# Kernel tuning notes

Measured on AMD Instinct MI355X. Metric: run time of the kernel, lower is better.

## Reference

```python
import jax, jax.numpy as jnp
import numpy as np
import math

SCALE = math.sqrt(256.0)

def setup_inputs() -> dict:
    key = jax.random.key(0)
    k1, k2, k3, k4, k5 = jax.random.split(key, 5)
    B, C, T, D = 8, 80, 2048, 256
    bound = 1.0 / math.sqrt(C)
    x = jax.random.normal(k1, (B, C, T), dtype=jnp.float32)
    Wk = jax.random.uniform(k2, (D, C), minval=-bound, maxval=bound, dtype=jnp.float32)
    bk = jax.random.uniform(k3, (D,), minval=-bound, maxval=bound, dtype=jnp.float32)
    Wq = jax.random.uniform(k4, (D, C), minval=-bound, maxval=bound, dtype=jnp.float32)
    bq = jax.random.uniform(k5, (D,), minval=-bound, maxval=bound, dtype=jnp.float32)
    return {"x": x, "Wk": Wk, "bk": bk, "Wq": Wq, "bq": bq}

def reference(x, Wk, bk, Wq, bq):
    # x: [B, C=80, T]; work in time-major layout [B, T, C]
    xt = jnp.swapaxes(x, 1, 2)                      # [B, T, C]
    K = xt @ Wk.T + bk                              # [B, T, 256]
    Q = xt @ Wq.T + bq                              # [B, T, 256]
    # softmax over last dim (dim=2 in torch) of K Q^T / sqrt(256)
    att = jax.nn.softmax(jnp.einsum('bid,bjd->bij', K, Q) / SCALE, axis=2)
    # original per-timestep loop is exactly att @ xt (values = raw input, no V proj)
    out = jnp.einsum('bij,bjc->bic', att, xt)       # [B, T, C]
    return jnp.swapaxes(out, 1, 2)                  # [B, C, T]
```

## Files before the change

kernel.cpp:

```cpp
#include <hip/hip_runtime.h>
#include <hip/hip_bf16.h>
#include <math.h>

typedef __bf16 bf16;
typedef __bf16 bf16x8 __attribute__((ext_vector_type(8)));
typedef float  f32x4  __attribute__((ext_vector_type(4)));
typedef float  f32x16 __attribute__((ext_vector_type(16)));
typedef uint32_t u32x4 __attribute__((ext_vector_type(4)));

#define MFMA16(a, b, c) __builtin_amdgcn_mfma_f32_16x16x32_bf16((a), (b), (c), 0, 0, 0)
#define MFMA32(a, b, c) __builtin_amdgcn_mfma_f32_32x32x16_bf16((a), (b), (c), 0, 0, 0)

typedef const uint32_t __attribute__((address_space(1)))* gq_t;
typedef uint32_t __attribute__((address_space(3)))* lq_t;

constexpr int B_ = 8, C_ = 80, T_ = 2048, D_ = 256;
constexpr int NS = 4;
constexpr float LOG2E_16 = 0.090169989f;

static __device__ inline uint32_t pkbf(float lo, float hi) {
  bf16 l = (bf16)lo, h = (bf16)hi;
  uint16_t lb = __builtin_bit_cast(uint16_t, l), hb = __builtin_bit_cast(uint16_t, h);
  return (uint32_t)lb | ((uint32_t)hb << 16);
}

constexpr int VF_TILE = 3 * 2 * 2 * 32 * 8;

__global__ __launch_bounds__(256) void proj_kernel(
    const float* __restrict__ x,
    const float* __restrict__ Wk,
    const float* __restrict__ bk,
    const float* __restrict__ Wq,
    const float* __restrict__ bq,
    bf16* __restrict__ Kb,
    bf16* __restrict__ Qb,
    bf16* __restrict__ Vf)
{
  const int t0   = blockIdx.x * 32;
  const int b    = blockIdx.y;
  const int tid  = threadIdx.x;
  const int w    = tid >> 6;
  const int lane = tid & 63;
  const int h    = lane >> 4;
  const int lr   = lane & 15;

  const float* xb = x + (size_t)b * C_ * T_;

  {
    bf16* vout = Vf + (size_t)(b * 64 + blockIdx.x) * VF_TILE;
    #pragma unroll
    for (int g = 0; g < 2; ++g) {
      int f = tid + g * 256;
      if (f < 384) {
        int il2 = f & 31, hi2 = (f >> 5) & 1, kj2 = (f >> 6) & 1, cb2 = f >> 7;
        int c = cb2 * 32 + il2;
        bf16x8 o;
        if (c < 80) {
          const float* sp = xb + (size_t)c * T_ + t0 + kj2 * 16 + hi2 * 8;
          f32x4 v0 = *reinterpret_cast<const f32x4*>(sp);
          f32x4 v1 = *reinterpret_cast<const f32x4*>(sp + 4);
          #pragma unroll
          for (int e = 0; e < 4; ++e) { o[e] = (bf16)v0[e]; o[e + 4] = (bf16)v1[e]; }
        } else {
          #pragma unroll
          for (int e = 0; e < 8; ++e) o[e] = (bf16)0.f;
        }
        *reinterpret_cast<bf16x8*>(vout + f * 8) = o;
      }
    }
  }

  bf16x8 afrag[2][3];
  #pragma unroll
  for (int ib = 0; ib < 2; ++ib) {
    int t = t0 + ib * 16 + lr;
    #pragma unroll
    for (int ks = 0; ks < 3; ++ks) {
      bf16x8 v;
      #pragma unroll
      for (int e = 0; e < 8; ++e) {
        int c = ks * 32 + h * 8 + e;
        float val;
        if (c < 80)       val = xb[c * T_ + t];
        else if (c == 80) val = 1.0f;
        else              val = 0.0f;
        v[e] = (bf16)val;
      }
      afrag[ib][ks] = v;
    }
  }

  const int nb0 = w * 4;
  #pragma unroll
  for (int mat = 0; mat < 2; ++mat) {
    const float* W    = mat ? Wq : Wk;
    const float* bias = mat ? bq : bk;
    bf16* outp        = mat ? Qb : Kb;

    f32x4 acc[2][4];
    #pragma unroll
    for (int ib = 0; ib < 2; ++ib)
      #pragma unroll
      for (int nb = 0; nb < 4; ++nb)
        acc[ib][nb] = f32x4{0.f, 0.f, 0.f, 0.f};

    #pragma unroll
    for (int nb = 0; nb < 4; ++nb) {
      int d = (nb0 + nb) * 16 + lr;
      #pragma unroll
      for (int ks = 0; ks < 3; ++ks) {
        bf16x8 bv;
        #pragma unroll
        for (int e = 0; e < 8; ++e) {
          int c = ks * 32 + h * 8 + e;
          float val;
          if (c < 80)       val = W[d * C_ + c];
          else if (c == 80) val = bias[d];
          else              val = 0.0f;
          bv[e] = (bf16)val;
        }
        #pragma unroll
        for (int ib = 0; ib < 2; ++ib)
          acc[ib][nb] = MFMA16(afrag[ib][ks], bv, acc[ib][nb]);
      }
    }

    #pragma unroll
    for (int ib = 0; ib < 2; ++ib)
      #pragma unroll
      for (int nb = 0; nb < 4; ++nb) {
        int d = (nb0 + nb) * 16 + lr;
        #pragma unroll
        for (int r = 0; r < 4; ++r) {
          int t = t0 + ib * 16 + h * 4 + r;
          outp[(size_t)(b * T_ + t) * D_ + d] = (bf16)acc[ib][nb][r];
        }
      }
  }
}

__global__ __launch_bounds__(256, 2) void attn_kernel(
    const bf16* __restrict__ Kb,
    const bf16* __restrict__ Qb,
    const bf16* __restrict__ Vf,
    float* __restrict__ Opart,
    float* __restrict__ mpart,
    float* __restrict__ lpart)
{
  constexpr int BN = 32, NT = T_ / BN;
  constexpr int JT_PER = NT / NS;
  __shared__ bf16 qlds[2][BN * D_];
  __shared__ bf16 vlds[2][VF_TILE];

  const int flat = blockIdx.x;
  const int b    = flat & 7;
  const int rem  = flat >> 3;
  const int it   = rem & 15;
  const int s    = rem >> 4;
  const int i0   = it * 128;

  const int tid  = threadIdx.x;
  const int w    = tid >> 6;
  const int lane = tid & 63;
  const int il   = lane & 31;
  const int hi   = lane >> 5;
  const int iw   = i0 + w * 32;

  const bf16* Kbase = Kb + (size_t)b * T_ * D_;
  const bf16* Qbase = Qb + (size_t)b * T_ * D_;
  const bf16* Vbase = Vf + (size_t)b * 64 * VF_TILE;

  bf16x8 kf[16];
  {
    const bf16* kp = Kbase + (size_t)(iw + il) * D_ + hi * 8;
    #pragma unroll
    for (int ks = 0; ks < 16; ++ks)
      kf[ks] = *reinterpret_cast<const bf16x8*>(kp + ks * 16);
  }

  f32x16 oacc[3];
  #pragma unroll
  for (int cb = 0; cb < 3; ++cb)
    #pragma unroll
    for (int r = 0; r < 16; ++r) oacc[cb][r] = 0.f;
  float m_run = -INFINITY, l_run = 0.f;

  auto stage = [&](int jt, int buf) {
    #pragma unroll
    for (int q = 0; q < 4; ++q) {
      int f = tid + 256 * q;
      int j = f >> 5, c = f & 31;
      const bf16* src = Qbase + (size_t)(jt * BN + j) * D_ + ((c ^ j) << 3);
      __builtin_amdgcn_global_load_lds((gq_t)src,
          (lq_t)&qlds[buf][(q * 256 + w * 64) * 8], 16, 0, 0);
    }
    const bf16* vsrc = Vbase + (size_t)jt * VF_TILE;
    __builtin_amdgcn_global_load_lds((gq_t)(vsrc + (size_t)tid * 8),
        (lq_t)&vlds[buf][(w * 64) * 8], 16, 0, 0);
    if (w < 2)
      __builtin_amdgcn_global_load_lds((gq_t)(vsrc + (size_t)(256 + tid) * 8),
          (lq_t)&vlds[buf][(256 + w * 64) * 8], 16, 0, 0);
  };

  const int jt0 = s * JT_PER, jtend = jt0 + JT_PER;

  stage(jt0, 0);
  asm volatile("s_waitcnt vmcnt(0)" ::: "memory");
  __syncthreads();

  int cur = 0;
  for (int jt = jt0; jt < jtend; ++jt, cur ^= 1) {
    if (jt + 1 < jtend) stage(jt + 1, cur ^ 1);

    bf16x8 vf[3][2];
    #pragma unroll
    for (int cb = 0; cb < 3; ++cb)
      #pragma unroll
      for (int kj = 0; kj < 2; ++kj)
        vf[cb][kj] = *reinterpret_cast<const bf16x8*>(
            &vlds[cur][(size_t)(((cb * 2 + kj) * 2 + hi) * 32 + il) * 8]);

    f32x16 sacc;
    #pragma unroll
    for (int r = 0; r < 16; ++r) sacc[r] = 0.f;
    __builtin_amdgcn_s_setprio(1);
    #pragma unroll
    for (int ks = 0; ks < 16; ++ks) {
      bf16x8 qa = *reinterpret_cast<const bf16x8*>(
          &qlds[cur][il * 256 + (((hi + 2 * ks) ^ il) << 3)]);
      sacc = MFMA32(qa, kf[ks], sacc);
    }
    __builtin_amdgcn_s_setprio(0);

    float p16[16];
    #pragma unroll
    for (int r = 0; r < 16; ++r) p16[r] = sacc[r];
    float mx01 = fmaxf(p16[0], p16[1]),  mx23 = fmaxf(p16[2], p16[3]);
    float mx45 = fmaxf(p16[4], p16[5]),  mx67 = fmaxf(p16[6], p16[7]);
    float mx89 = fmaxf(p16[8], p16[9]),  mxab = fmaxf(p16[10], p16[11]);
    float mxcd = fmaxf(p16[12], p16[13]), mxef = fmaxf(p16[14], p16[15]);
    float mx = fmaxf(fmaxf(fmaxf(mx01, mx23), fmaxf(mx45, mx67)),
                     fmaxf(fmaxf(mx89, mxab), fmaxf(mxcd, mxef)));
    mx = fmaxf(mx, __shfl_xor(mx, 32));

    if (!__all(mx <= m_run + 48.f)) {
      float mnew  = fmaxf(m_run, mx);
      float alpha = exp2f((m_run - mnew) * LOG2E_16);
      m_run = mnew;
      l_run *= alpha;
      #pragma unroll
      for (int cb = 0; cb < 3; ++cb)
        #pragma unroll
        for (int r = 0; r < 16; ++r) oacc[cb][r] *= alpha;
    }
    float rs = 0.f;
    #pragma unroll
    for (int r = 0; r < 16; ++r) {
      p16[r] = exp2f((p16[r] - m_run) * LOG2E_16);
      rs += p16[r];
    }
    l_run += rs;

    uint32_t a0 = pkbf(p16[0],  p16[1]),  a1 = pkbf(p16[2],  p16[3]);
    uint32_t c0 = pkbf(p16[4],  p16[5]),  c1 = pkbf(p16[6],  p16[7]);
    uint32_t a2 = pkbf(p16[8],  p16[9]),  a3 = pkbf(p16[10], p16[11]);
    uint32_t c2 = pkbf(p16[12], p16[13]), c3 = pkbf(p16[14], p16[15]);
    uint32_t a0s = __shfl_xor(a0, 32), a1s = __shfl_xor(a1, 32);
    uint32_t c0s = __shfl_xor(c0, 32), c1s = __shfl_xor(c1, 32);
    uint32_t a2s = __shfl_xor(a2, 32), a3s = __shfl_xor(a3, 32);
    uint32_t c2s = __shfl_xor(c2, 32), c3s = __shfl_xor(c3, 32);
    const bool hh = (hi != 0);
    u32x4 pb0 = { hh ? c0s : a0, hh ? c1s : a1, hh ? c0 : a0s, hh ? c1 : a1s };
    u32x4 pb1 = { hh ? c2s : a2, hh ? c3s : a3, hh ? c2 : a2s, hh ? c3 : a3s };
    bf16x8 pbf0 = __builtin_bit_cast(bf16x8, pb0);
    bf16x8 pbf1 = __builtin_bit_cast(bf16x8, pb1);

    __builtin_amdgcn_s_setprio(1);
    #pragma unroll
    for (int cb = 0; cb < 3; ++cb) {
      oacc[cb] = MFMA32(vf[cb][0], pbf0, oacc[cb]);
      oacc[cb] = MFMA32(vf[cb][1], pbf1, oacc[cb]);
    }
    __builtin_amdgcn_s_setprio(0);

    asm volatile("s_waitcnt vmcnt(0)" ::: "memory");
    __syncthreads();
  }

  l_run += __shfl_xor(l_run, 32);

  float* ob = Opart + (size_t)(s * B_ + b) * C_ * T_;
  #pragma unroll
  for (int cb = 0; cb < 3; ++cb)
    #pragma unroll
    for (int r = 0; r < 16; ++r) {
      if (cb < 2 || r < 8) {
        int c = cb * 32 + (r & 3) + 8 * (r >> 2) + 4 * hi;
        ob[(size_t)c * T_ + iw + il] = oacc[cb][r];
      }
    }
  if (lane < 32) {
    mpart[(size_t)(s * B_ + b) * T_ + iw + il] = m_run;
    lpart[(size_t)(s * B_ + b) * T_ + iw + il] = l_run;
  }
}

__global__ __launch_bounds__(256) void merge_kernel(
    const float* __restrict__ Opart,
    const float* __restrict__ mpart,
    const float* __restrict__ lpart,
    float* __restrict__ out)
{
  const int b      = blockIdx.y;
  const int tid    = threadIdx.x;
  const int slot   = tid & 15;
  const int cstrip = tid >> 4;
  const int t4     = blockIdx.x * 64 + slot * 4;

  f32x4 m[NS], e[NS];
  f32x4 mmax;
  #pragma unroll
  for (int s2 = 0; s2 < NS; ++s2)
    m[s2] = *reinterpret_cast<const f32x4*>(&mpart[(size_t)(s2 * B_ + b) * T_ + t4]);
  #pragma unroll
  for (int r = 0; r < 4; ++r) {
    mmax[r] = m[0][r];
    #pragma unroll
    for (int s2 = 1; s2 < NS; ++s2) mmax[r] = fmaxf(mmax[r], m[s2][r]);
  }
  f32x4 lsum = f32x4{0.f, 0.f, 0.f, 0.f};
  #pragma unroll
  for (int s2 = 0; s2 < NS; ++s2) {
    f32x4 lv = *reinterpret_cast<const f32x4*>(&lpart[(size_t)(s2 * B_ + b) * T_ + t4]);
    #pragma unroll
    for (int r = 0; r < 4; ++r) e[s2][r] = exp2f((m[s2][r] - mmax[r]) * LOG2E_16);
    lsum += e[s2] * lv;
  }
  f32x4 inv;
  #pragma unroll
  for (int r = 0; r < 4; ++r) inv[r] = 1.0f / lsum[r];

  #pragma unroll
  for (int cc = 0; cc < 5; ++cc) {
    const int c = cstrip * 5 + cc;
    f32x4 acc = f32x4{0.f, 0.f, 0.f, 0.f};
    #pragma unroll
    for (int s2 = 0; s2 < NS; ++s2)
      acc += *reinterpret_cast<const f32x4*>(
                 &Opart[((size_t)(s2 * B_ + b) * C_ + c) * T_ + t4]) * e[s2];
    *reinterpret_cast<f32x4*>(&out[((size_t)b * C_ + c) * T_ + t4]) = acc * inv;
  }
}

extern "C" void kernel_launch(void* const* d_in, const int* in_sizes, int n_in,
                              void* d_out, int out_size, void* d_ws, size_t ws_size,
                              hipStream_t stream) {
  (void)in_sizes; (void)n_in; (void)out_size; (void)ws_size;
  const float* x  = (const float*)d_in[0];
  const float* Wk = (const float*)d_in[1];
  const float* bk = (const float*)d_in[2];
  const float* Wq = (const float*)d_in[3];
  const float* bq = (const float*)d_in[4];
  float* out = (float*)d_out;

  char* ws = (char*)d_ws;
  const size_t MB = 1024 * 1024;
  bf16*  Kb    = (bf16*)(ws);
  bf16*  Qb    = (bf16*)(ws + 8 * MB);
  bf16*  Vf    = (bf16*)(ws + 16 * MB);
  float* Opart = (float*)(ws + 19 * MB);
  float* mpart = (float*)(ws + 41 * MB);
  float* lpart = (float*)(ws + 42 * MB);

  dim3 blk(256);
  dim3 g1(T_ / 32, B_);
  proj_kernel<<<g1, blk, 0, stream>>>(x, Wk, bk, Wq, bq, Kb, Qb, Vf);
  attn_kernel<<<dim3(16 * NS * B_), blk, 0, stream>>>(Kb, Qb, Vf, Opart, mpart, lpart);
  dim3 g3(T_ / 64, B_);
  merge_kernel<<<g3, blk, 0, stream>>>(Opart, mpart, lpart, out);
}
```

Before: 69.40 us.

## Pre-convert weights to bf16, load V fragments directly, stagger key-tile order

Adds a tiny kernel that converts Wk/Wq plus bias into a padded bf16 layout, so the projection kernel does vector loads instead of scalar fp32 gathers with branches. The attention kernel no longer stages V tiles through LDS and reads V fragments straight from global memory. It also rotates the key-tile iteration order per query block to spread concurrent reads across tiles. The costs are an extra kernel launch and V loads that are no longer prefetched, which exposes their global latency inside the loop.

```diff
diff --git a/kernel.cpp b/kernel.cpp
--- a/kernel.cpp
+++ b/kernel.cpp
@@ -26,12 +26,32 @@
 
 constexpr int VF_TILE = 3 * 2 * 2 * 32 * 8;
 
+__global__ __launch_bounds__(256) void wconv_kernel(
+    const float* __restrict__ Wk, const float* __restrict__ bk,
+    const float* __restrict__ Wq, const float* __restrict__ bq,
+    bf16* __restrict__ Wbf)
+{
+  const int mat = blockIdx.x, d = threadIdx.x;
+  const float* W    = mat ? Wq : Wk;
+  const float* bias = mat ? bq : bk;
+  bf16* row = Wbf + (size_t)(mat * 256 + d) * 96;
+  const float bv = bias[d];
+  #pragma unroll
+  for (int c8 = 0; c8 < 12; ++c8) {
+    bf16x8 o;
+    #pragma unroll
+    for (int e = 0; e < 8; ++e) {
+      int c = c8 * 8 + e;
+      float v = (c < 80) ? W[d * C_ + c] : (c == 80 ? bv : 0.f);
+      o[e] = (bf16)v;
+    }
+    *reinterpret_cast<bf16x8*>(row + c8 * 8) = o;
+  }
+}
+
 __global__ __launch_bounds__(256) void proj_kernel(
     const float* __restrict__ x,
-    const float* __restrict__ Wk,
-    const float* __restrict__ bk,
-    const float* __restrict__ Wq,
-    const float* __restrict__ bq,
+    const bf16* __restrict__ Wbf,
     bf16* __restrict__ Kb,
     bf16* __restrict__ Qb,
     bf16* __restrict__ Vf)
@@ -93,9 +113,7 @@
   const int nb0 = w * 4;
   #pragma unroll
   for (int mat = 0; mat < 2; ++mat) {
-    const float* W    = mat ? Wq : Wk;
-    const float* bias = mat ? bq : bk;
-    bf16* outp        = mat ? Qb : Kb;
+    bf16* outp = mat ? Qb : Kb;
 
     f32x4 acc[2][4];
     #pragma unroll
@@ -107,18 +125,10 @@
     #pragma unroll
     for (int nb = 0; nb < 4; ++nb) {
       int d = (nb0 + nb) * 16 + lr;
+      const bf16* wrow = Wbf + (size_t)(mat * 256 + d) * 96;
       #pragma unroll
       for (int ks = 0; ks < 3; ++ks) {
-        bf16x8 bv;
-        #pragma unroll
-        for (int e = 0; e < 8; ++e) {
-          int c = ks * 32 + h * 8 + e;
-          float val;
-          if (c < 80)       val = W[d * C_ + c];
-          else if (c == 80) val = bias[d];
-          else              val = 0.0f;
-          bv[e] = (bf16)val;
-        }
+        bf16x8 bv = *reinterpret_cast<const bf16x8*>(wrow + ks * 32 + h * 8);
         #pragma unroll
         for (int ib = 0; ib < 2; ++ib)
           acc[ib][nb] = MFMA16(afrag[ib][ks], bv, acc[ib][nb]);
@@ -150,7 +160,6 @@
   constexpr int BN = 32, NT = T_ / BN;
   constexpr int JT_PER = NT / NS;
   __shared__ bf16 qlds[2][BN * D_];
-  __shared__ bf16 vlds[2][VF_TILE];
 
   const int flat = blockIdx.x;
   const int b    = flat & 7;
@@ -185,6 +194,10 @@
     for (int r = 0; r < 16; ++r) oacc[cb][r] = 0.f;
   float m_run = -INFINITY, l_run = 0.f;
 
+  const int jt0 = s * JT_PER, jtend = jt0 + JT_PER;
+  const int off = (it & 3) * 4;
+  auto jmap = [&](int t) { return jt0 + ((t - jt0 + off) & (JT_PER - 1)); };
+
   auto stage = [&](int jt, int buf) {
     #pragma unroll
     for (int q = 0; q < 4; ++q) {
@@ -194,31 +207,24 @@
       __builtin_amdgcn_global_load_lds((gq_t)src,
           (lq_t)&qlds[buf][(q * 256 + w * 64) * 8], 16, 0, 0);
     }
-    const bf16* vsrc = Vbase + (size_t)jt * VF_TILE;
-    __builtin_amdgcn_global_load_lds((gq_t)(vsrc + (size_t)tid * 8),
-        (lq_t)&vlds[buf][(w * 64) * 8], 16, 0, 0);
-    if (w < 2)
-      __builtin_amdgcn_global_load_lds((gq_t)(vsrc + (size_t)(256 + tid) * 8),
-          (lq_t)&vlds[buf][(256 + w * 64) * 8], 16, 0, 0);
   };
 
-  const int jt0 = s * JT_PER, jtend = jt0 + JT_PER;
-
-  stage(jt0, 0);
+  stage(jmap(jt0), 0);
   asm volatile("s_waitcnt vmcnt(0)" ::: "memory");
   __syncthreads();
 
   int cur = 0;
-  for (int jt = jt0; jt < jtend; ++jt, cur ^= 1) {
-    if (jt + 1 < jtend) stage(jt + 1, cur ^ 1);
-
+  for (int t = jt0; t < jtend; ++t, cur ^= 1) {
+    const int jt = jmap(t);
+    if (t + 1 < jtend) stage(jmap(t + 1), cur ^ 1);
+
+    const bf16* vt = Vbase + (size_t)jt * VF_TILE + lane * 8;
     bf16x8 vf[3][2];
     #pragma unroll
     for (int cb = 0; cb < 3; ++cb)
       #pragma unroll
       for (int kj = 0; kj < 2; ++kj)
-        vf[cb][kj] = *reinterpret_cast<const bf16x8*>(
-            &vlds[cur][(size_t)(((cb * 2 + kj) * 2 + hi) * 32 + il) * 8]);
+        vf[cb][kj] = *reinterpret_cast<const bf16x8*>(vt + (cb * 2 + kj) * 512);
 
     f32x16 sacc;
     #pragma unroll
@@ -368,13 +374,15 @@
   bf16*  Kb    = (bf16*)(ws);
   bf16*  Qb    = (bf16*)(ws + 8 * MB);
   bf16*  Vf    = (bf16*)(ws + 16 * MB);
-  float* Opart = (float*)(ws + 19 * MB);
-  float* mpart = (float*)(ws + 41 * MB);
-  float* lpart = (float*)(ws + 42 * MB);
+  bf16*  Wbf   = (bf16*)(ws + 19 * MB);
+  float* Opart = (float*)(ws + 20 * MB);
+  float* mpart = (float*)(ws + 42 * MB);
+  float* lpart = (float*)(ws + 43 * MB);
 
   dim3 blk(256);
+  wconv_kernel<<<dim3(2), blk, 0, stream>>>(Wk, bk, Wq, bq, Wbf);
   dim3 g1(T_ / 32, B_);
-  proj_kernel<<<g1, blk, 0, stream>>>(x, Wk, bk, Wq, bq, Kb, Qb, Vf);
+  proj_kernel<<<g1, blk, 0, stream>>>(x, Wbf, Kb, Qb, Vf);
   attn_kernel<<<dim3(16 * NS * B_), blk, 0, stream>>>(Kb, Qb, Vf, Opart, mpart, lpart);
   dim3 g3(T_ / 64, B_);
   merge_kernel<<<g3, blk, 0, stream>>>(Opart, mpart, lpart, out);
```

After: 66.62 us. -4.0%, faster.
